# Kernel optimization log

Measured on AMD Instinct MI355X. Metric: run time of the kernel, lower is better.

## Reference

```python
import jax, jax.numpy as jnp
import numpy as np

TOKEN_VOCAB = 512   # token id range used for packing ngram tuples into ints
VOCAB_SIZE = 50000  # max ngram vocab per size (ngram_to_size values)
NGRAM_SIZES = (2, 3)
OOV_ID = 0
ID_OFFSET = 4       # vocab ids start at 4 (idx + 4 in _get_top_ngrams)


def _make_table(rng, n):
    # Build a sorted, unique packed-key table emulating the dict produced by
    # _get_top_ngrams: {ngram_tuple: idx+4}. Keys packed base-TOKEN_VOCAB.
    cand = rng.integers(0, TOKEN_VOCAB, size=(VOCAB_SIZE * 3, n), dtype=np.int64)
    packed = np.zeros(cand.shape[0], dtype=np.int64)
    for j in range(n):
        packed = packed * TOKEN_VOCAB + cand[:, j]
    uniq = np.unique(packed)[:VOCAB_SIZE]
    keys = np.sort(uniq)
    vals = np.arange(keys.shape[0], dtype=np.int64) + ID_OFFSET
    return jnp.asarray(keys), jnp.asarray(vals)


def setup_inputs() -> dict:
    key = jax.random.key(0)
    x = jax.random.randint(key, (256, 8192), 0, TOKEN_VOCAB, dtype=jnp.int64)
    rng = np.random.default_rng(0)
    keys2, vals2 = _make_table(rng, 2)
    keys3, vals3 = _make_table(rng, 3)
    return {"x": x, "keys2": keys2, "vals2": vals2, "keys3": keys3, "vals3": vals3}


def _encode_ngram_ids(x, keys, vals, n):
    # Left-pad with 0 by (n-1), sliding windows of length n per position,
    # pack each window into a single int key, then sorted-table lookup
    # (semantically equal to lookup_table.get(tuple(window), 0)).
    B, S = x.shape
    padded = jnp.pad(x, ((0, 0), (n - 1, 0)))  # [B, S+n-1]
    packed = jnp.zeros((B, S), dtype=jnp.int64)
    for j in range(n):  # tiny fixed loop over window offset
        packed = packed * TOKEN_VOCAB + padded[:, j:j + S]
    pos = jnp.clip(jnp.searchsorted(keys, packed.ravel()), 0, keys.shape[0] - 1)
    hit = keys[pos] == packed.ravel()
    ids = jnp.where(hit, vals[pos], OOV_ID)
    return ids.reshape(B, S)


def reference(x, keys2, vals2, keys3, vals3):
    tables = {2: (keys2, vals2), 3: (keys3, vals3)}
    per_n = [_encode_ngram_ids(x, *tables[n], n) for n in NGRAM_SIZES]
    return jnp.stack(per_n, axis=0)  # [n_sizes, B, S]
```

## Files before the change

kernel.cpp:

```cpp
#include <hip/hip_runtime.h>


#define TOKEN_VOCAB 512
#define D2_ENTRIES (TOKEN_VOCAB * TOKEN_VOCAB)
#define SHIFT3 10
#define NBUCKET3 (1 << 17)

__global__ void build_direct2(const int* __restrict__ keys2,
                              const int* __restrict__ vals2, int K2,
                              int* __restrict__ direct2) {
    int i = blockIdx.x * blockDim.x + threadIdx.x;
    if (i < K2) direct2[keys2[i]] = vals2[i];
}

__global__ void build_start3(const int* __restrict__ keys3, int K3,
                             int* __restrict__ start3) {
    int b = blockIdx.x * blockDim.x + threadIdx.x;
    if (b > NBUCKET3) return;
    int target = b << SHIFT3;
    int lo = 0, hi = K3;
    while (lo < hi) {
        int mid = (lo + hi) >> 1;
        if (keys3[mid] < target) lo = mid + 1; else hi = mid;
    }
    start3[b] = lo;
}

__global__ void pack_meta(const int* __restrict__ start3,
                          unsigned* __restrict__ meta) {
    int b = blockIdx.x * blockDim.x + threadIdx.x;
    if (b >= NBUCKET3) return;
    int st = start3[b];
    int cnt = start3[b + 1] - st;
    meta[b] = ((unsigned)st << 11) | (unsigned)cnt;
}

__global__ void __launch_bounds__(256)
ngram_main(const int* __restrict__ x,
           const int* __restrict__ direct2,
           const unsigned* __restrict__ meta,
           const int* __restrict__ keys3,
           const int* __restrict__ vals3,
           int* __restrict__ out, int total, int S) {
    int base = (blockIdx.x * blockDim.x + threadIdx.x) * 4;
    if (base >= total) return;
    int s = base & (S - 1);
    const int4 cur = *(const int4*)(x + base);
    int tm1 = (s >= 1) ? x[base - 1] : 0;
    int tm2 = (s >= 1) ? x[base - 2] : 0;
    int t[6] = {tm2, tm1, cur.x, cur.y, cur.z, cur.w};

    int o2[4], k3v[4];
    unsigned m[4];
    #pragma unroll
    for (int j = 0; j < 4; ++j) {
        int k2 = t[j + 1] * TOKEN_VOCAB + t[j + 2];
        int k3 = (t[j] * TOKEN_VOCAB + t[j + 1]) * TOKEN_VOCAB + t[j + 2];
        k3v[j] = k3;
        o2[j] = direct2[k2];
        m[j] = meta[k3 >> SHIFT3];
    }
    int o3[4];
    #pragma unroll
    for (int j = 0; j < 4; ++j) {
        int v = 0;
        int cnt = (int)(m[j] & 2047u);
        if (cnt) {
            int p = (int)(m[j] >> 11);
            for (int e = 0; e < cnt; ++e) {
                int kv = keys3[p + e];
                if (kv >= k3v[j]) { if (kv == k3v[j]) v = vals3[p + e]; break; }
            }
        }
        o3[j] = v;
    }
    *(int4*)(out + base)         = make_int4(o2[0], o2[1], o2[2], o2[3]);
    *(int4*)(out + total + base) = make_int4(o3[0], o3[1], o3[2], o3[3]);
}

__device__ __forceinline__ int table_lookup(const int* __restrict__ keys,
                                            const int* __restrict__ vals,
                                            int K, int packed) {
    int lo = 0, hi = K;
    while (lo < hi) {
        int mid = (lo + hi) >> 1;
        if (keys[mid] < packed) lo = mid + 1; else hi = mid;
    }
    int pos = lo < (K - 1) ? lo : (K - 1);
    return (keys[pos] == packed) ? vals[pos] : 0;
}

__global__ void ngram_encode_kernel(const int* __restrict__ x,
                                    const int* __restrict__ keys2,
                                    const int* __restrict__ vals2, int K2,
                                    const int* __restrict__ keys3,
                                    const int* __restrict__ vals3, int K3,
                                    int* __restrict__ out, int total, int S) {
    int idx = blockIdx.x * blockDim.x + threadIdx.x;
    if (idx >= total) return;
    int s = idx & (S - 1);
    int t0 = x[idx];
    int t1 = (s >= 1) ? x[idx - 1] : 0;
    int t2 = (s >= 2) ? x[idx - 2] : 0;
    int k2 = t1 * TOKEN_VOCAB + t0;
    int k3 = (t2 * TOKEN_VOCAB + t1) * TOKEN_VOCAB + t0;
    out[idx]         = table_lookup(keys2, vals2, K2, k2);
    out[total + idx] = table_lookup(keys3, vals3, K3, k3);
}

extern "C" void kernel_launch(void* const* d_in, const int* in_sizes, int n_in,
                              void* d_out, int out_size, void* d_ws, size_t ws_size,
                              hipStream_t stream) {
    const int* x     = (const int*)d_in[0];
    const int* keys2 = (const int*)d_in[1];
    const int* vals2 = (const int*)d_in[2];
    const int* keys3 = (const int*)d_in[3];
    const int* vals3 = (const int*)d_in[4];
    int* out = (int*)d_out;

    const int total = in_sizes[0];
    const int S = 8192;
    const int K2 = in_sizes[1];
    const int K3 = in_sizes[3];

    int*      direct2 = (int*)d_ws;
    int*      start3  = direct2 + D2_ENTRIES;
    unsigned* meta    = (unsigned*)(start3 + NBUCKET3 + 1);
    const size_t ws_needed = (size_t)(D2_ENTRIES + NBUCKET3 + 1 + NBUCKET3) * 4;

    if (ws_size >= ws_needed) {
        hipMemsetAsync(direct2, 0, (size_t)D2_ENTRIES * 4, stream);
        build_direct2<<<(K2 + 255) / 256, 256, 0, stream>>>(keys2, vals2, K2, direct2);
        build_start3<<<(NBUCKET3 + 1 + 255) / 256, 256, 0, stream>>>(keys3, K3, start3);
        pack_meta<<<(NBUCKET3 + 255) / 256, 256, 0, stream>>>(start3, meta);

        const int elems = total / 4;
        ngram_main<<<(elems + 255) / 256, 256, 0, stream>>>(
            x, direct2, meta, keys3, vals3, out, total, S);
    } else {
        ngram_encode_kernel<<<(total + 255) / 256, 256, 0, stream>>>(
            x, keys2, vals2, K2, keys3, vals3, K3, out, total, S);
    }
}
```

Baseline: 102.1 us.

## Fuse table builds into one kernel, shrink 2-gram table to u16, process 8 tokens/thread

Replaces the memset plus three build kernels with a single build_all kernel. It fills a dense 2-gram table by binary search over keys2 and computes the 3-gram bucket metadata with two lower_bound searches per bucket. The 2-gram direct table is stored as unsigned short, halving its footprint so more of it stays in cache. The main kernel now handles 8 tokens per thread instead of 4, which adds memory-level parallelism. The cost is a binary search per 2-gram table entry instead of a scatter, and values must fit in 16 bits.

```diff
diff --git a/kernel.cpp b/kernel.cpp
--- a/kernel.cpp
+++ b/kernel.cpp
@@ -2,67 +2,67 @@
 
 
 #define TOKEN_VOCAB 512
-#define D2_ENTRIES (TOKEN_VOCAB * TOKEN_VOCAB)
+#define D2_ENTRIES (1 << 18)
 #define SHIFT3 10
 #define NBUCKET3 (1 << 17)
 
-__global__ void build_direct2(const int* __restrict__ keys2,
-                              const int* __restrict__ vals2, int K2,
-                              int* __restrict__ direct2) {
-    int i = blockIdx.x * blockDim.x + threadIdx.x;
-    if (i < K2) direct2[keys2[i]] = vals2[i];
-}
-
-__global__ void build_start3(const int* __restrict__ keys3, int K3,
-                             int* __restrict__ start3) {
-    int b = blockIdx.x * blockDim.x + threadIdx.x;
-    if (b > NBUCKET3) return;
-    int target = b << SHIFT3;
-    int lo = 0, hi = K3;
+__device__ __forceinline__ int lower_bound_dev(const int* __restrict__ a,
+                                               int n, int target) {
+    int lo = 0, hi = n;
     while (lo < hi) {
         int mid = (lo + hi) >> 1;
-        if (keys3[mid] < target) lo = mid + 1; else hi = mid;
+        if (a[mid] < target) lo = mid + 1; else hi = mid;
     }
-    start3[b] = lo;
-}
-
-__global__ void pack_meta(const int* __restrict__ start3,
-                          unsigned* __restrict__ meta) {
-    int b = blockIdx.x * blockDim.x + threadIdx.x;
-    if (b >= NBUCKET3) return;
-    int st = start3[b];
-    int cnt = start3[b + 1] - st;
-    meta[b] = ((unsigned)st << 11) | (unsigned)cnt;
+    return lo;
 }
 
 __global__ void __launch_bounds__(256)
-ngram_main(const int* __restrict__ x,
-           const int* __restrict__ direct2,
-           const unsigned* __restrict__ meta,
-           const int* __restrict__ keys3,
-           const int* __restrict__ vals3,
-           int* __restrict__ out, int total, int S) {
-    int base = (blockIdx.x * blockDim.x + threadIdx.x) * 4;
+build_all(const int* __restrict__ keys2, const int* __restrict__ vals2, int K2,
+          const int* __restrict__ keys3, int K3,
+          unsigned short* __restrict__ d2, unsigned* __restrict__ meta) {
+    int i = blockIdx.x * blockDim.x + threadIdx.x;
+    if (i < D2_ENTRIES) {
+        int lo = lower_bound_dev(keys2, K2, i);
+        unsigned short v = 0;
+        if (lo < K2 && keys2[lo] == i) v = (unsigned short)vals2[lo];
+        d2[i] = v;
+    }
+    if (i < NBUCKET3) {
+        int lo = lower_bound_dev(keys3, K3, i << SHIFT3);
+        int hi = lower_bound_dev(keys3, K3, (i + 1) << SHIFT3);
+        meta[i] = ((unsigned)lo << 11) | (unsigned)(hi - lo);
+    }
+}
+
+__global__ void __launch_bounds__(256)
+main8(const int* __restrict__ x,
+      const unsigned short* __restrict__ d2,
+      const unsigned* __restrict__ meta,
+      const int* __restrict__ keys3,
+      const int* __restrict__ vals3,
+      int* __restrict__ out, int total, int S) {
+    int base = (blockIdx.x * blockDim.x + threadIdx.x) * 8;
     if (base >= total) return;
     int s = base & (S - 1);
-    const int4 cur = *(const int4*)(x + base);
+    const int4 ca = *(const int4*)(x + base);
+    const int4 cb = *(const int4*)(x + base + 4);
     int tm1 = (s >= 1) ? x[base - 1] : 0;
     int tm2 = (s >= 1) ? x[base - 2] : 0;
-    int t[6] = {tm2, tm1, cur.x, cur.y, cur.z, cur.w};
+    int t[10] = {tm2, tm1, ca.x, ca.y, ca.z, ca.w, cb.x, cb.y, cb.z, cb.w};
 
-    int o2[4], k3v[4];
-    unsigned m[4];
+    int o2[8], k3v[8];
+    unsigned m[8];
     #pragma unroll
-    for (int j = 0; j < 4; ++j) {
+    for (int j = 0; j < 8; ++j) {
         int k2 = t[j + 1] * TOKEN_VOCAB + t[j + 2];
         int k3 = (t[j] * TOKEN_VOCAB + t[j + 1]) * TOKEN_VOCAB + t[j + 2];
         k3v[j] = k3;
-        o2[j] = direct2[k2];
+        o2[j] = (int)d2[k2];
         m[j] = meta[k3 >> SHIFT3];
     }
-    int o3[4];
+    int o3[8];
     #pragma unroll
-    for (int j = 0; j < 4; ++j) {
+    for (int j = 0; j < 8; ++j) {
         int v = 0;
         int cnt = (int)(m[j] & 2047u);
         if (cnt) {
@@ -74,8 +74,10 @@
         }
         o3[j] = v;
     }
-    *(int4*)(out + base)         = make_int4(o2[0], o2[1], o2[2], o2[3]);
-    *(int4*)(out + total + base) = make_int4(o3[0], o3[1], o3[2], o3[3]);
+    *(int4*)(out + base)             = make_int4(o2[0], o2[1], o2[2], o2[3]);
+    *(int4*)(out + base + 4)         = make_int4(o2[4], o2[5], o2[6], o2[7]);
+    *(int4*)(out + total + base)     = make_int4(o3[0], o3[1], o3[2], o3[3]);
+    *(int4*)(out + total + base + 4) = make_int4(o3[4], o3[5], o3[6], o3[7]);
 }
 
 __device__ __forceinline__ int table_lookup(const int* __restrict__ keys,
@@ -123,20 +125,16 @@
     const int K2 = in_sizes[1];
     const int K3 = in_sizes[3];
 
-    int*      direct2 = (int*)d_ws;
-    int*      start3  = direct2 + D2_ENTRIES;
-    unsigned* meta    = (unsigned*)(start3 + NBUCKET3 + 1);
-    const size_t ws_needed = (size_t)(D2_ENTRIES + NBUCKET3 + 1 + NBUCKET3) * 4;
+    unsigned short* d2   = (unsigned short*)d_ws;
+    unsigned*       meta = (unsigned*)(d2 + D2_ENTRIES);
+    const size_t ws_needed = (size_t)D2_ENTRIES * 2 + (size_t)NBUCKET3 * 4;
 
     if (ws_size >= ws_needed) {
-        hipMemsetAsync(direct2, 0, (size_t)D2_ENTRIES * 4, stream);
-        build_direct2<<<(K2 + 255) / 256, 256, 0, stream>>>(keys2, vals2, K2, direct2);
-        build_start3<<<(NBUCKET3 + 1 + 255) / 256, 256, 0, stream>>>(keys3, K3, start3);
-        pack_meta<<<(NBUCKET3 + 255) / 256, 256, 0, stream>>>(start3, meta);
-
-        const int elems = total / 4;
-        ngram_main<<<(elems + 255) / 256, 256, 0, stream>>>(
-            x, direct2, meta, keys3, vals3, out, total, S);
+        build_all<<<(D2_ENTRIES + 255) / 256, 256, 0, stream>>>(
+            keys2, vals2, K2, keys3, K3, d2, meta);
+        const int threads_main = total / 8;
+        main8<<<(threads_main + 255) / 256, 256, 0, stream>>>(
+            x, d2, meta, keys3, vals3, out, total, S);
     } else {
         ngram_encode_kernel<<<(total + 255) / 256, 256, 0, stream>>>(
             x, keys2, vals2, K2, keys3, vals3, K3, out, total, S);
```

Result: no change. 103.0 us (+0.9%).
